# Optimization experiments

Measured on AMD Instinct MI355X. Metric: run time of the kernel, lower is better.

Reference implementation:

```python
import jax, jax.numpy as jnp
import numpy as np

N = 100_000          # nodes
E = 600_000          # directed edges, stored in reverse pairs (2i <-> 2i+1)
D_NODE = 128
D_EDGE = 16
UNITS = 128
EDGE_STEPS = 4
NODE_STEPS = 4


def setup_inputs() -> dict:
    key = jax.random.key(0)
    ks = jax.random.split(key, 10)
    s = 0.05
    # undirected pairs -> both directions so every edge has a reverse edge
    u = jax.random.randint(ks[0], (E // 2,), 0, N, dtype=jnp.int32)
    v = jax.random.randint(ks[1], (E // 2,), 0, N, dtype=jnp.int32)
    edge_src = jnp.stack([u, v], axis=1).reshape(-1)  # [E]
    edge_dst = jnp.stack([v, u], axis=1).reshape(-1)  # [E]
    edge_rev = (jnp.arange(E, dtype=jnp.int32) ^ 1)   # reverse-edge index
    return dict(
        node_feature=jax.random.normal(ks[2], (N, D_NODE), jnp.float32),
        edge_feature=jax.random.normal(ks[3], (E, D_EDGE), jnp.float32),
        W_init=jax.random.normal(ks[4], (D_NODE + D_EDGE, UNITS), jnp.float32) * s,
        b_init=jnp.zeros((UNITS,), jnp.float32),
        W_edge=jax.random.normal(ks[5], (EDGE_STEPS, UNITS, UNITS), jnp.float32) * s,
        b_edge=jnp.zeros((EDGE_STEPS, UNITS), jnp.float32),
        W_gin0=jax.random.normal(ks[6], (D_NODE + UNITS, UNITS), jnp.float32) * s,
        W_gin=jax.random.normal(ks[7], (NODE_STEPS - 1, UNITS, UNITS), jnp.float32) * s,
        b_gin=jnp.zeros((NODE_STEPS, UNITS), jnp.float32),
        eps=jnp.zeros((NODE_STEPS,), jnp.float32),
        edge_src=edge_src,
        edge_dst=edge_dst,
        edge_rev=edge_rev,
    )


def reference(node_feature, edge_feature, W_init, b_init, W_edge, b_edge,
              W_gin0, W_gin, b_gin, eps, edge_src, edge_dst, edge_rev):
    relu = jax.nn.relu
    seg = lambda x: jax.ops.segment_sum(x, edge_dst, num_segments=N)

    # ---- EdgeConv stack (D-MPNN directed edge message passing) ----
    # initial edge state: act(W [x_src || e])
    h = relu(jnp.concatenate([node_feature[edge_src], edge_feature], axis=-1)
             @ W_init + b_init)                                  # [E, U]
    for t in range(EDGE_STEPS):
        agg = seg(h)                                             # [N, U] incoming sums
        m = agg[edge_src] - h[edge_rev]                          # exclude reverse edge
        h = relu(h + m @ W_edge[t] + b_edge[t])                  # residual edge update

    # ---- NodeReadout: sum incoming edge states per node ----
    readout = seg(h)                                             # [N, U]
    x = jnp.concatenate([node_feature, readout], axis=-1)        # [N, D_NODE + U]

    # ---- GINConv stack (use_edge_features=False) ----
    for t in range(NODE_STEPS):
        agg = seg(x[edge_src])                                   # [N, d] neighbor sum
        W = W_gin0 if t == 0 else W_gin[t - 1]
        x = relu(((1.0 + eps[t]) * x + agg) @ W + b_gin[t])      # [N, U]

    return x, h
```

## Files before the change

kernel.cpp:

```cpp
#include <hip/hip_runtime.h>

#define N_NODES 100000
#define N_EDGES 600000
#define SCAN_NB ((N_NODES + 255) / 256)

typedef unsigned short u16;
typedef __attribute__((ext_vector_type(8))) short short8v;
typedef __attribute__((ext_vector_type(4))) short short4v;
typedef __attribute__((ext_vector_type(4))) float f32x4;
typedef __attribute__((ext_vector_type(8))) __bf16 bf16x8v;

__device__ __forceinline__ u16 f2bf(float f) {
  unsigned u = __builtin_bit_cast(unsigned, f);
  unsigned r = (u + 0x7fffu + ((u >> 16) & 1u)) >> 16;
  return (u16)r;
}
__device__ __forceinline__ float bf2f(u16 v) {
  unsigned u = ((unsigned)v) << 16;
  return __builtin_bit_cast(float, u);
}
__device__ __forceinline__ short8v shfl_xor4_v(short8v v) {
  int4 iv = __builtin_bit_cast(int4, v);
  iv.x = __shfl_xor(iv.x, 4, 64);
  iv.y = __shfl_xor(iv.y, 4, 64);
  iv.z = __shfl_xor(iv.z, 4, 64);
  iv.w = __shfl_xor(iv.w, 4, 64);
  return __builtin_bit_cast(short8v, iv);
}

__global__ __launch_bounds__(256) void convert_nf_kernel(const float* __restrict__ nf,
                                                         u16* __restrict__ nfbf) {
  size_t idx = ((size_t)blockIdx.x * 256 + threadIdx.x) * 8;
  if (idx >= (size_t)N_NODES * 128) return;
  float4 a = *(const float4*)(nf + idx);
  float4 b = *(const float4*)(nf + idx + 4);
  short8v o = {(short)f2bf(a.x), (short)f2bf(a.y), (short)f2bf(a.z), (short)f2bf(a.w),
               (short)f2bf(b.x), (short)f2bf(b.y), (short)f2bf(b.z), (short)f2bf(b.w)};
  *(short8v*)(nfbf + idx) = o;
}

__global__ void hist_kernel(const int* __restrict__ dst, int* __restrict__ cnt) {
  int e = blockIdx.x * 256 + threadIdx.x;
  if (e < N_EDGES) atomicAdd(&cnt[dst[e]], 1);
}

__global__ __launch_bounds__(256) void scan1_kernel(int* __restrict__ cnt,
                                                    int* __restrict__ off,
                                                    int* __restrict__ blk) {
  __shared__ int s[256];
  int i = blockIdx.x * 256 + threadIdx.x;
  int v = (i < N_NODES) ? cnt[i] : 0;
  if (i < N_NODES) cnt[i] = 0;
  s[threadIdx.x] = v;
  __syncthreads();
  for (int d = 1; d < 256; d <<= 1) {
    int t = (threadIdx.x >= d) ? s[threadIdx.x - d] : 0;
    __syncthreads();
    s[threadIdx.x] += t;
    __syncthreads();
  }
  if (i < N_NODES) off[i] = s[threadIdx.x] - v;
  if (threadIdx.x == 255) blk[blockIdx.x] = s[255];
}

__global__ __launch_bounds__(512) void scan2_kernel(int* __restrict__ blk) {
  __shared__ int s[512];
  int v = (threadIdx.x < SCAN_NB) ? blk[threadIdx.x] : 0;
  s[threadIdx.x] = v;
  __syncthreads();
  for (int d = 1; d < 512; d <<= 1) {
    int t = (threadIdx.x >= d) ? s[threadIdx.x - d] : 0;
    __syncthreads();
    s[threadIdx.x] += t;
    __syncthreads();
  }
  if (threadIdx.x < SCAN_NB) blk[threadIdx.x] = s[threadIdx.x] - v;
}

__global__ __launch_bounds__(256) void scan3_kernel(int* __restrict__ off,
                                                    const int* __restrict__ blk) {
  int i = blockIdx.x * 256 + threadIdx.x;
  if (i < N_NODES) off[i] += blk[blockIdx.x];
  if (i == 0) off[N_NODES] = N_EDGES;
}

__global__ void fill_kernel(const int* __restrict__ dst, const int* __restrict__ src,
                            const int* __restrict__ off, int* __restrict__ cur,
                            int* __restrict__ csr_e, int* __restrict__ csr_s) {
  int e = blockIdx.x * 256 + threadIdx.x;
  if (e < N_EDGES) {
    int d = dst[e];
    int p = off[d] + atomicAdd(&cur[d], 1);
    csr_e[p] = e;
    csr_s[p] = src[e];
  }
}

__global__ __launch_bounds__(256) void segsum_hbf_kernel(const u16* __restrict__ hbf,
                                                         const int* __restrict__ off,
                                                         const int* __restrict__ csr_e,
                                                         u16* __restrict__ aggb) {
  int node = blockIdx.x * 4 + (threadIdx.x >> 6);
  int l = threadIdx.x & 63;
  int p0 = off[node], p1 = off[node + 1];
  int deg = p1 - p0;
  int e_l = (l < deg) ? csr_e[p0 + min(l, deg - 1)] : 0;
  float a0 = 0.f, a1 = 0.f;
  int jmax = min(deg, 64);
  for (int j = 0; j < jmax; ++j) {
    int e = __shfl(e_l, j, 64);
    unsigned u = *(const unsigned*)(hbf + (size_t)e * 128 + 2 * l);
    a0 += __builtin_bit_cast(float, u << 16);
    a1 += __builtin_bit_cast(float, u & 0xffff0000u);
  }
  for (int p = p0 + 64; p < p1; ++p) {
    int e = csr_e[p];
    unsigned u = *(const unsigned*)(hbf + (size_t)e * 128 + 2 * l);
    a0 += __builtin_bit_cast(float, u << 16);
    a1 += __builtin_bit_cast(float, u & 0xffff0000u);
  }
  unsigned o = (unsigned)f2bf(a0) | (((unsigned)f2bf(a1)) << 16);
  *(unsigned*)(aggb + (size_t)node * 128 + 2 * l) = o;
}

__global__ __launch_bounds__(256) void segsum_readout_kernel(const u16* __restrict__ hbf,
                                                             const int* __restrict__ off,
                                                             const int* __restrict__ csr_e,
                                                             u16* __restrict__ readout) {
  int node = blockIdx.x * 4 + (threadIdx.x >> 6);
  int l = threadIdx.x & 63;
  int p0 = off[node], p1 = off[node + 1];
  int deg = p1 - p0;
  int e_l = (l < deg) ? csr_e[p0 + min(l, deg - 1)] : 0;
  float a0 = 0.f, a1 = 0.f;
  int jmax = min(deg, 64);
  for (int j = 0; j < jmax; ++j) {
    int e = __shfl(e_l, j, 64);
    unsigned u = __builtin_nontemporal_load((const unsigned*)(hbf + (size_t)e * 128 + 2 * l));
    a0 += __builtin_bit_cast(float, u << 16);
    a1 += __builtin_bit_cast(float, u & 0xffff0000u);
  }
  for (int p = p0 + 64; p < p1; ++p) {
    int e = csr_e[p];
    unsigned u = __builtin_nontemporal_load((const unsigned*)(hbf + (size_t)e * 128 + 2 * l));
    a0 += __builtin_bit_cast(float, u << 16);
    a1 += __builtin_bit_cast(float, u & 0xffff0000u);
  }
  unsigned o = (unsigned)f2bf(a0) | (((unsigned)f2bf(a1)) << 16);
  *(unsigned*)(readout + (size_t)node * 128 + 2 * l) = o;
}

#define PREP_INIT 0
#define PREP_EDGE 1
#define PREP_GIN0 2
#define PREP_GINX 3
#define EPI_BR  1
#define EPI_ABR 2

template<int KSTEPS, int PREPM, int EPIM, int OUTBF>
__global__ __launch_bounds__(256, 3) void mfma_gemm(
    const float* __restrict__ Wf, int KREAL,
    const float* __restrict__ bias,
    const void* __restrict__ P0,
    const void* __restrict__ P1,
    const int* __restrict__ srcIdx,
    const int* __restrict__ csr_off,
    const int* __restrict__ csr_s,
    const float* __restrict__ epsp,
    float* __restrict__ OutF32,
    void* __restrict__ Out, int numRows) {
  constexpr int RS = KSTEPS * 32 + 8;
  constexpr bool WLATE = (KSTEPS >= 8);
  __shared__ short amem[64 * RS];
  const int t = threadIdx.x;
  const int l = t & 63;
  const int w = t >> 6;
  const int g = l >> 4;
  const int n0 = l & 15;
  const int base = blockIdx.x * 64;

  short8v wf[KSTEPS][2];
  auto load_w = [&]() {
    #pragma unroll
    for (int s = 0; s < KSTEPS; ++s) {
      #pragma unroll
      for (int ct = 0; ct < 2; ++ct) {
        short8v v;
        #pragma unroll
        for (int j = 0; j < 8; ++j) {
          int k = 32 * s + 8 * g + j;
          float wv = (k < KREAL) ? Wf[(size_t)k * 128 + (2 * w + ct) * 16 + n0] : 0.f;
          v[j] = (short)f2bf(wv);
        }
        wf[s][ct] = v;
      }
    }
  };
  if constexpr (!WLATE) load_w();

  float bb[2];
  #pragma unroll
  for (int ct = 0; ct < 2; ++ct) bb[ct] = bias[(2 * w + ct) * 16 + n0];
  float alpha = 0.f;
  if constexpr (PREPM == PREP_GIN0 || PREPM == PREP_GINX) alpha = 1.f + epsp[0];

  short8v hself[4];

  if constexpr (PREPM == PREP_INIT) {
    const int i = t >> 2, q = t & 3;
    const int row = base + i;
    const int sn = srcIdx[row];
    const u16* nrow = (const u16*)P0 + (size_t)sn * 128 + q * 32;
    #pragma unroll
    for (int c = 0; c < 4; ++c)
      *(short8v*)(&amem[i * RS + q * 32 + 8 * c]) = *(const short8v*)(nrow + 8 * c);
    #pragma unroll
    for (int z = 0; z < 2; ++z) {
      int col = 128 + (2 * q + z) * 4;
      short4v o = {0, 0, 0, 0};
      if (col < 144) {
        float4 vv = *(const float4*)((const float*)P1 + (size_t)row * 16 + (col - 128));
        o = {(short)f2bf(vv.x), (short)f2bf(vv.y), (short)f2bf(vv.z), (short)f2bf(vv.w)};
      }
      *(short4v*)(&amem[i * RS + col]) = o;
    }
  } else if constexpr (PREPM == PREP_EDGE) {
    const int i = t >> 2, q = t & 3;
    const int row = base + i;
    const int sn = srcIdx[row];
    const u16* arow = (const u16*)P0 + (size_t)sn * 128 + q * 32;
    const u16* hrow = (const u16*)P1 + (size_t)row * 128 + q * 32;
    short8v av[4];
    #pragma unroll
    for (int c = 0; c < 4; ++c) av[c] = *(const short8v*)(arow + 8 * c);
    #pragma unroll
    for (int c = 0; c < 4; ++c) hself[c] = *(const short8v*)(hrow + 8 * c);
    #pragma unroll
    for (int c = 0; c < 4; ++c) {
      short8v hrev = shfl_xor4_v(hself[c]);
      short8v o;
      #pragma unroll
      for (int j = 0; j < 8; ++j)
        o[j] = (short)f2bf(bf2f((u16)av[c][j]) - bf2f((u16)hrev[j]));
      *(short8v*)(&amem[i * RS + q * 32 + 8 * c]) = o;
    }
  } else if constexpr (PREPM == PREP_GIN0) {
    const int i2 = t >> 3, q = t & 7;
    #pragma unroll
    for (int half = 0; half < 2; ++half) {
      const int r = i2 + 32 * half;
      const int row = base + r;
      const int n = (row < numRows) ? row : (numRows - 1);
      const int p0 = csr_off[n], p1 = csr_off[n + 1];
      const u16* basep = (q < 4) ? (const u16*)P0 : (const u16*)P1;
      const int coff = (q < 4) ? 32 * q : 32 * (q - 4);
      float acc[32];
      const u16* self = basep + (size_t)n * 128 + coff;
      #pragma unroll
      for (int c8 = 0; c8 < 4; ++c8) {
        short8v v = *(const short8v*)(self + 8 * c8);
        #pragma unroll
        for (int j = 0; j < 8; ++j) acc[8 * c8 + j] = alpha * bf2f((u16)v[j]);
      }
      for (int p = p0; p < p1; ++p) {
        const u16* nb = basep + (size_t)csr_s[p] * 128 + coff;
        #pragma unroll
        for (int c8 = 0; c8 < 4; ++c8) {
          short8v v = *(const short8v*)(nb + 8 * c8);
          #pragma unroll
          for (int j = 0; j < 8; ++j) acc[8 * c8 + j] += bf2f((u16)v[j]);
        }
      }
      #pragma unroll
      for (int c4 = 0; c4 < 8; ++c4) {
        short4v o = {(short)f2bf(acc[4 * c4 + 0]), (short)f2bf(acc[4 * c4 + 1]),
                     (short)f2bf(acc[4 * c4 + 2]), (short)f2bf(acc[4 * c4 + 3])};
        *(short4v*)(&amem[r * RS + 32 * q + 4 * c4]) = o;
      }
    }
  } else {
    const int i = t >> 2, q = t & 3;
    const int row = base + i;
    const int n = (row < numRows) ? row : (numRows - 1);
    const int p0 = csr_off[n], p1 = csr_off[n + 1];
    float acc[32];
    const u16* self = (const u16*)P0 + (size_t)n * 128 + 32 * q;
    #pragma unroll
    for (int c8 = 0; c8 < 4; ++c8) {
      short8v v = *(const short8v*)(self + 8 * c8);
      #pragma unroll
      for (int j = 0; j < 8; ++j) acc[8 * c8 + j] = alpha * bf2f((u16)v[j]);
    }
    for (int p = p0; p < p1; ++p) {
      const u16* nb = (const u16*)P0 + (size_t)csr_s[p] * 128 + 32 * q;
      #pragma unroll
      for (int c8 = 0; c8 < 4; ++c8) {
        short8v v = *(const short8v*)(nb + 8 * c8);
        #pragma unroll
        for (int j = 0; j < 8; ++j) acc[8 * c8 + j] += bf2f((u16)v[j]);
      }
    }
    #pragma unroll
    for (int c4 = 0; c4 < 8; ++c4) {
      short4v o = {(short)f2bf(acc[4 * c4 + 0]), (short)f2bf(acc[4 * c4 + 1]),
                   (short)f2bf(acc[4 * c4 + 2]), (short)f2bf(acc[4 * c4 + 3])};
      *(short4v*)(&amem[i * RS + 32 * q + 4 * c4]) = o;
    }
  }
  __syncthreads();
  if constexpr (WLATE) load_w();

  f32x4 acc[4][2];
  #pragma unroll
  for (int rt = 0; rt < 4; ++rt)
    #pragma unroll
    for (int ct = 0; ct < 2; ++ct) acc[rt][ct] = (f32x4){0.f, 0.f, 0.f, 0.f};
  #pragma unroll
  for (int s = 0; s < KSTEPS; ++s) {
    bf16x8v af[4];
    #pragma unroll
    for (int rt = 0; rt < 4; ++rt) {
      short8v araw = *(const short8v*)(&amem[(16 * rt + n0) * RS + s * 32 + g * 8]);
      af[rt] = __builtin_bit_cast(bf16x8v, araw);
    }
    #pragma unroll
    for (int rt = 0; rt < 4; ++rt)
      #pragma unroll
      for (int ct = 0; ct < 2; ++ct)
        acc[rt][ct] = __builtin_amdgcn_mfma_f32_16x16x32_bf16(
            af[rt], __builtin_bit_cast(bf16x8v, wf[s][ct]), acc[rt][ct], 0, 0, 0);
  }

  if constexpr (EPIM == EPI_ABR) {
    __syncthreads();
    {
      const int i = t >> 2, q = t & 3;
      #pragma unroll
      for (int c = 0; c < 4; ++c)
        *(short8v*)(&amem[i * RS + q * 32 + 8 * c]) = hself[c];
    }
    __syncthreads();
  }

  if constexpr (OUTBF) {
    if constexpr (EPIM != EPI_ABR) __syncthreads();
    #pragma unroll
    for (int rt = 0; rt < 4; ++rt) {
      #pragma unroll
      for (int ct = 0; ct < 2; ++ct) {
        #pragma unroll
        for (int r = 0; r < 4; ++r) {
          int lrow = 16 * rt + 4 * g + r;
          int lcol = (2 * w + ct) * 16 + n0;
          float o = acc[rt][ct][r];
          if constexpr (EPIM == EPI_ABR) o += bf2f((u16)amem[lrow * RS + lcol]);
          o = fmaxf(o + bb[ct], 0.f);
          if constexpr (OUTBF == 2)
            __builtin_nontemporal_store(o, &OutF32[(size_t)(base + lrow) * 128 + lcol]);
          amem[lrow * RS + lcol] = (short)f2bf(o);
        }
      }
    }
    __syncthreads();
    {
      const int i = t >> 2, q = t & 3;
      const int row = base + i;
      if (row < numRows) {
        u16* orow = (u16*)Out + (size_t)row * 128 + q * 32;
        #pragma unroll
        for (int c = 0; c < 4; ++c)
          *(short8v*)(orow + 8 * c) = *(const short8v*)(&amem[i * RS + q * 32 + 8 * c]);
      }
    }
  } else {
    #pragma unroll
    for (int rt = 0; rt < 4; ++rt) {
      #pragma unroll
      for (int ct = 0; ct < 2; ++ct) {
        #pragma unroll
        for (int r = 0; r < 4; ++r) {
          int row = base + 16 * rt + 4 * g + r;
          if (row < numRows) {
            int lrow = 16 * rt + 4 * g + r;
            int lcol = (2 * w + ct) * 16 + n0;
            float o = acc[rt][ct][r];
            if constexpr (EPIM == EPI_ABR) o += bf2f((u16)amem[lrow * RS + lcol]);
            o = fmaxf(o + bb[ct], 0.f);
            __builtin_nontemporal_store(o, &((float*)Out)[(size_t)row * 128 + lcol]);
          }
        }
      }
    }
  }
}

extern "C" void kernel_launch(void* const* d_in, const int* in_sizes, int n_in,
                              void* d_out, int out_size, void* d_ws, size_t ws_size,
                              hipStream_t stream) {
  const float* nf     = (const float*)d_in[0];
  const float* ef     = (const float*)d_in[1];
  const float* W_init = (const float*)d_in[2];
  const float* b_init = (const float*)d_in[3];
  const float* W_edge = (const float*)d_in[4];
  const float* b_edge = (const float*)d_in[5];
  const float* W_gin0 = (const float*)d_in[6];
  const float* W_gin  = (const float*)d_in[7];
  const float* b_gin  = (const float*)d_in[8];
  const float* eps    = (const float*)d_in[9];
  const int* esrc     = (const int*)d_in[10];
  const int* edst     = (const int*)d_in[11];

  float* xout  = (float*)d_out;
  float* h_out = xout + (size_t)N_NODES * 128;

  const size_t NB = (size_t)N_NODES * 128 * 2;
  const size_t EB = (size_t)N_EDGES * 128 * 2;
  char* wsb = (char*)d_ws;
  u16* aggbf   = (u16*)wsb;
  u16* xbf1    = (u16*)wsb;
  u16* hbf     = (u16*)(wsb + NB);
  u16* readout = (u16*)(wsb + NB + EB);
  u16* xbf0    = (u16*)(wsb + 2 * NB + EB);
  u16* nfbf    = (u16*)(wsb + 3 * NB + EB);
  int* csr_off = (int*)(wsb + 4 * NB + EB);
  int* cursor  = csr_off + (N_NODES + 1);
  int* csr_e   = cursor + N_NODES;
  int* csr_s   = csr_e + N_EDGES;
  int* blk     = csr_s + N_EDGES;

  convert_nf_kernel<<<(N_NODES * 128 / 8 + 255) / 256, 256, 0, stream>>>(nf, nfbf);

  hipMemsetAsync(cursor, 0, N_NODES * sizeof(int), stream);
  hist_kernel<<<(N_EDGES + 255) / 256, 256, 0, stream>>>(edst, cursor);
  scan1_kernel<<<SCAN_NB, 256, 0, stream>>>(cursor, csr_off, blk);
  scan2_kernel<<<1, 512, 0, stream>>>(blk);
  scan3_kernel<<<SCAN_NB, 256, 0, stream>>>(csr_off, blk);
  fill_kernel<<<(N_EDGES + 255) / 256, 256, 0, stream>>>(edst, esrc, csr_off, cursor, csr_e, csr_s);

  const int ETILES = N_EDGES / 64;
  const int NTILES = (N_NODES + 63) / 64;

  mfma_gemm<5, PREP_INIT, EPI_BR, 1><<<ETILES, 256, 0, stream>>>(
      W_init, 144, b_init, nfbf, ef, esrc, nullptr, nullptr, nullptr, nullptr, hbf, N_EDGES);

  for (int t = 0; t < 3; ++t) {
    segsum_hbf_kernel<<<N_NODES / 4, 256, 0, stream>>>(hbf, csr_off, csr_e, aggbf);
    mfma_gemm<4, PREP_EDGE, EPI_ABR, 1><<<ETILES, 256, 0, stream>>>(
        W_edge + (size_t)t * 128 * 128, 128, b_edge + (size_t)t * 128,
        aggbf, hbf, esrc, nullptr, nullptr, nullptr, nullptr, hbf, N_EDGES);
  }
  segsum_hbf_kernel<<<N_NODES / 4, 256, 0, stream>>>(hbf, csr_off, csr_e, aggbf);
  mfma_gemm<4, PREP_EDGE, EPI_ABR, 2><<<ETILES, 256, 0, stream>>>(
      W_edge + (size_t)3 * 128 * 128, 128, b_edge + (size_t)3 * 128,
      aggbf, hbf, esrc, nullptr, nullptr, nullptr, h_out, hbf, N_EDGES);

  segsum_readout_kernel<<<N_NODES / 4, 256, 0, stream>>>(hbf, csr_off, csr_e, readout);

  mfma_gemm<8, PREP_GIN0, EPI_BR, 1><<<NTILES, 256, 0, stream>>>(
      W_gin0, 256, b_gin, nfbf, readout, nullptr, csr_off, csr_s, eps, nullptr, xbf0, N_NODES);

  mfma_gemm<4, PREP_GINX, EPI_BR, 1><<<NTILES, 256, 0, stream>>>(
      W_gin, 128, b_gin + 128, xbf0, nullptr, nullptr, csr_off, csr_s, eps + 1, nullptr, xbf1, N_NODES);
  mfma_gemm<4, PREP_GINX, EPI_BR, 1><<<NTILES, 256, 0, stream>>>(
      W_gin + (size_t)128 * 128, 128, b_gin + 256, xbf1, nullptr, nullptr, csr_off, csr_s, eps + 2, nullptr, xbf0, N_NODES);
  mfma_gemm<4, PREP_GINX, EPI_BR, 0><<<NTILES, 256, 0, stream>>>(
      W_gin + (size_t)2 * 128 * 128, 128, b_gin + 384, xbf0, nullptr, nullptr, csr_off, csr_s, eps + 3, nullptr, xout, N_NODES);

  (void)in_sizes; (void)n_in; (void)out_size; (void)ws_size;
}
```

Baseline: 1.178 ms.

## Pre-convert weights to bf16, make GEMM blocks persistent, interleave node feature with readout

A new kernel converts all weight matrices once into a transposed bf16 blob, so each GEMM block loads its weight fragments as vector loads instead of doing strided fp32 loads and conversions. The GEMM kernels now loop over several 64-row tiles per block (5 for edges, 3 for nodes), which spreads the weight-load and bias setup over more rows. Node features and the readout are stored together in one 256-wide row, so the first GIN step gathers 32-column slices of a single interleaved row. The cost is fewer blocks, which lowers parallelism and latency hiding, plus one extra small kernel launch.

```diff
diff --git a/kernel.cpp b/kernel.cpp
--- a/kernel.cpp
+++ b/kernel.cpp
@@ -3,6 +3,12 @@
 #define N_NODES 100000
 #define N_EDGES 600000
 #define SCAN_NB ((N_NODES + 255) / 256)
+
+#define WOFF_I  0
+#define WOFF_E  20480
+#define WOFF_G0 86016
+#define WOFF_G  118784
+#define WTOTAL  167936
 
 typedef unsigned short u16;
 typedef __attribute__((ext_vector_type(8))) short short8v;
@@ -29,14 +35,44 @@
 }
 
 __global__ __launch_bounds__(256) void convert_nf_kernel(const float* __restrict__ nf,
-                                                         u16* __restrict__ nfbf) {
+                                                         u16* __restrict__ nfro) {
   size_t idx = ((size_t)blockIdx.x * 256 + threadIdx.x) * 8;
   if (idx >= (size_t)N_NODES * 128) return;
   float4 a = *(const float4*)(nf + idx);
   float4 b = *(const float4*)(nf + idx + 4);
   short8v o = {(short)f2bf(a.x), (short)f2bf(a.y), (short)f2bf(a.z), (short)f2bf(a.w),
                (short)f2bf(b.x), (short)f2bf(b.y), (short)f2bf(b.z), (short)f2bf(b.w)};
-  *(short8v*)(nfbf + idx) = o;
+  size_t row = idx >> 7, col = idx & 127;
+  *(short8v*)(nfro + row * 256 + col) = o;
+}
+
+__global__ __launch_bounds__(256) void convert_w_kernel(const float* __restrict__ Wi,
+                                                        const float* __restrict__ We,
+                                                        const float* __restrict__ Wg0,
+                                                        const float* __restrict__ Wg,
+                                                        u16* __restrict__ out) {
+  int e = blockIdx.x * 256 + threadIdx.x;
+  if (e >= WTOTAL) return;
+  float v;
+  if (e < WOFF_E) {
+    int col = e / 160, k = e % 160;
+    v = (k < 144) ? Wi[(size_t)k * 128 + col] : 0.f;
+  } else if (e < WOFF_G0) {
+    int r = e - WOFF_E;
+    int m = r / 16384; r %= 16384;
+    int col = r / 128, k = r % 128;
+    v = We[(size_t)m * 16384 + (size_t)k * 128 + col];
+  } else if (e < WOFF_G) {
+    int r = e - WOFF_G0;
+    int col = r / 256, k = r % 256;
+    v = Wg0[(size_t)k * 128 + col];
+  } else {
+    int r = e - WOFF_G;
+    int m = r / 16384; r %= 16384;
+    int col = r / 128, k = r % 128;
+    v = Wg[(size_t)m * 16384 + (size_t)k * 128 + col];
+  }
+  out[e] = f2bf(v);
 }
 
 __global__ void hist_kernel(const int* __restrict__ dst, int* __restrict__ cnt) {
@@ -126,7 +162,7 @@
 __global__ __launch_bounds__(256) void segsum_readout_kernel(const u16* __restrict__ hbf,
                                                              const int* __restrict__ off,
                                                              const int* __restrict__ csr_e,
-                                                             u16* __restrict__ readout) {
+                                                             u16* __restrict__ ro) {
   int node = blockIdx.x * 4 + (threadIdx.x >> 6);
   int l = threadIdx.x & 63;
   int p0 = off[node], p1 = off[node + 1];
@@ -147,7 +183,7 @@
     a1 += __builtin_bit_cast(float, u & 0xffff0000u);
   }
   unsigned o = (unsigned)f2bf(a0) | (((unsigned)f2bf(a1)) << 16);
-  *(unsigned*)(readout + (size_t)node * 128 + 2 * l) = o;
+  *(unsigned*)(ro + (size_t)node * 256 + 2 * l) = o;
 }
 
 #define PREP_INIT 0
@@ -157,9 +193,9 @@
 #define EPI_BR  1
 #define EPI_ABR 2
 
-template<int KSTEPS, int PREPM, int EPIM, int OUTBF>
+template<int KSTEPS, int PREPM, int EPIM, int OUTBF, int TPB>
 __global__ __launch_bounds__(256, 3) void mfma_gemm(
-    const float* __restrict__ Wf, int KREAL,
+    const u16* __restrict__ Wt,
     const float* __restrict__ bias,
     const void* __restrict__ P0,
     const void* __restrict__ P1,
@@ -177,24 +213,14 @@
   const int w = t >> 6;
   const int g = l >> 4;
   const int n0 = l & 15;
-  const int base = blockIdx.x * 64;
 
   short8v wf[KSTEPS][2];
   auto load_w = [&]() {
     #pragma unroll
-    for (int s = 0; s < KSTEPS; ++s) {
-      #pragma unroll
-      for (int ct = 0; ct < 2; ++ct) {
-        short8v v;
-        #pragma unroll
-        for (int j = 0; j < 8; ++j) {
-          int k = 32 * s + 8 * g + j;
-          float wv = (k < KREAL) ? Wf[(size_t)k * 128 + (2 * w + ct) * 16 + n0] : 0.f;
-          v[j] = (short)f2bf(wv);
-        }
-        wf[s][ct] = v;
-      }
-    }
+    for (int s = 0; s < KSTEPS; ++s)
+      #pragma unroll
+      for (int ct = 0; ct < 2; ++ct)
+        wf[s][ct] = *(const short8v*)(Wt + (size_t)((2 * w + ct) * 16 + n0) * (KSTEPS * 32) + 32 * s + 8 * g);
   };
   if constexpr (!WLATE) load_w();
 
@@ -204,58 +230,88 @@
   float alpha = 0.f;
   if constexpr (PREPM == PREP_GIN0 || PREPM == PREP_GINX) alpha = 1.f + epsp[0];
 
-  short8v hself[4];
-
-  if constexpr (PREPM == PREP_INIT) {
-    const int i = t >> 2, q = t & 3;
-    const int row = base + i;
-    const int sn = srcIdx[row];
-    const u16* nrow = (const u16*)P0 + (size_t)sn * 128 + q * 32;
-    #pragma unroll
-    for (int c = 0; c < 4; ++c)
-      *(short8v*)(&amem[i * RS + q * 32 + 8 * c]) = *(const short8v*)(nrow + 8 * c);
-    #pragma unroll
-    for (int z = 0; z < 2; ++z) {
-      int col = 128 + (2 * q + z) * 4;
-      short4v o = {0, 0, 0, 0};
-      if (col < 144) {
-        float4 vv = *(const float4*)((const float*)P1 + (size_t)row * 16 + (col - 128));
-        o = {(short)f2bf(vv.x), (short)f2bf(vv.y), (short)f2bf(vv.z), (short)f2bf(vv.w)};
-      }
-      *(short4v*)(&amem[i * RS + col]) = o;
-    }
-  } else if constexpr (PREPM == PREP_EDGE) {
-    const int i = t >> 2, q = t & 3;
-    const int row = base + i;
-    const int sn = srcIdx[row];
-    const u16* arow = (const u16*)P0 + (size_t)sn * 128 + q * 32;
-    const u16* hrow = (const u16*)P1 + (size_t)row * 128 + q * 32;
-    short8v av[4];
-    #pragma unroll
-    for (int c = 0; c < 4; ++c) av[c] = *(const short8v*)(arow + 8 * c);
-    #pragma unroll
-    for (int c = 0; c < 4; ++c) hself[c] = *(const short8v*)(hrow + 8 * c);
-    #pragma unroll
-    for (int c = 0; c < 4; ++c) {
-      short8v hrev = shfl_xor4_v(hself[c]);
-      short8v o;
-      #pragma unroll
-      for (int j = 0; j < 8; ++j)
-        o[j] = (short)f2bf(bf2f((u16)av[c][j]) - bf2f((u16)hrev[j]));
-      *(short8v*)(&amem[i * RS + q * 32 + 8 * c]) = o;
-    }
-  } else if constexpr (PREPM == PREP_GIN0) {
-    const int i2 = t >> 3, q = t & 7;
-    #pragma unroll
-    for (int half = 0; half < 2; ++half) {
-      const int r = i2 + 32 * half;
-      const int row = base + r;
+  for (int it = 0; it < TPB; ++it) {
+    const int base = (blockIdx.x * TPB + it) * 64;
+    short8v hself[4];
+
+    if constexpr (PREPM == PREP_INIT) {
+      const int i = t >> 2, q = t & 3;
+      const int row = base + i;
+      const int sn = srcIdx[row];
+      const u16* nrow = (const u16*)P0 + (size_t)sn * 256 + q * 32;
+      #pragma unroll
+      for (int c = 0; c < 4; ++c)
+        *(short8v*)(&amem[i * RS + q * 32 + 8 * c]) = *(const short8v*)(nrow + 8 * c);
+      #pragma unroll
+      for (int z = 0; z < 2; ++z) {
+        int col = 128 + (2 * q + z) * 4;
+        short4v o = {0, 0, 0, 0};
+        if (col < 144) {
+          f32x4 vv = __builtin_nontemporal_load(
+              (const f32x4*)((const float*)P1 + (size_t)row * 16 + (col - 128)));
+          o = {(short)f2bf(vv.x), (short)f2bf(vv.y), (short)f2bf(vv.z), (short)f2bf(vv.w)};
+        }
+        *(short4v*)(&amem[i * RS + col]) = o;
+      }
+    } else if constexpr (PREPM == PREP_EDGE) {
+      const int i = t >> 2, q = t & 3;
+      const int row = base + i;
+      const int sn = srcIdx[row];
+      const u16* arow = (const u16*)P0 + (size_t)sn * 128 + q * 32;
+      const u16* hrow = (const u16*)P1 + (size_t)row * 128 + q * 32;
+      short8v av[4];
+      #pragma unroll
+      for (int c = 0; c < 4; ++c) av[c] = *(const short8v*)(arow + 8 * c);
+      #pragma unroll
+      for (int c = 0; c < 4; ++c) hself[c] = *(const short8v*)(hrow + 8 * c);
+      #pragma unroll
+      for (int c = 0; c < 4; ++c) {
+        short8v hrev = shfl_xor4_v(hself[c]);
+        short8v o;
+        #pragma unroll
+        for (int j = 0; j < 8; ++j)
+          o[j] = (short)f2bf(bf2f((u16)av[c][j]) - bf2f((u16)hrev[j]));
+        *(short8v*)(&amem[i * RS + q * 32 + 8 * c]) = o;
+      }
+    } else if constexpr (PREPM == PREP_GIN0) {
+      const int i2 = t >> 3, q = t & 7;
+      #pragma unroll
+      for (int half = 0; half < 2; ++half) {
+        const int r = i2 + 32 * half;
+        const int row = base + r;
+        const int n = (row < numRows) ? row : (numRows - 1);
+        const int p0 = csr_off[n], p1 = csr_off[n + 1];
+        float acc[32];
+        const u16* self = (const u16*)P0 + (size_t)n * 256 + 32 * q;
+        #pragma unroll
+        for (int c8 = 0; c8 < 4; ++c8) {
+          short8v v = *(const short8v*)(self + 8 * c8);
+          #pragma unroll
+          for (int j = 0; j < 8; ++j) acc[8 * c8 + j] = alpha * bf2f((u16)v[j]);
+        }
+        for (int p = p0; p < p1; ++p) {
+          const u16* nb = (const u16*)P0 + (size_t)csr_s[p] * 256 + 32 * q;
+          #pragma unroll
+          for (int c8 = 0; c8 < 4; ++c8) {
+            short8v v = *(const short8v*)(nb + 8 * c8);
+            #pragma unroll
+            for (int j = 0; j < 8; ++j) acc[8 * c8 + j] += bf2f((u16)v[j]);
+          }
+        }
+        #pragma unroll
+        for (int c4 = 0; c4 < 8; ++c4) {
+          short4v o = {(short)f2bf(acc[4 * c4 + 0]), (short)f2bf(acc[4 * c4 + 1]),
+                       (short)f2bf(acc[4 * c4 + 2]), (short)f2bf(acc[4 * c4 + 3])};
+          *(short4v*)(&amem[r * RS + 32 * q + 4 * c4]) = o;
+        }
+      }
+    } else {
+      const int i = t >> 2, q = t & 3;
+      const int row = base + i;
       const int n = (row < numRows) ? row : (numRows - 1);
       const int p0 = csr_off[n], p1 = csr_off[n + 1];
-      const u16* basep = (q < 4) ? (const u16*)P0 : (const u16*)P1;
-      const int coff = (q < 4) ? 32 * q : 32 * (q - 4);
       float acc[32];
-      const u16* self = basep + (size_t)n * 128 + coff;
+      const u16* self = (const u16*)P0 + (size_t)n * 128 + 32 * q;
       #pragma unroll
       for (int c8 = 0; c8 < 4; ++c8) {
         short8v v = *(const short8v*)(self + 8 * c8);
@@ -263,7 +319,7 @@
         for (int j = 0; j < 8; ++j) acc[8 * c8 + j] = alpha * bf2f((u16)v[j]);
       }
       for (int p = p0; p < p1; ++p) {
-        const u16* nb = basep + (size_t)csr_s[p] * 128 + coff;
+        const u16* nb = (const u16*)P0 + (size_t)csr_s[p] * 128 + 32 * q;
         #pragma unroll
         for (int c8 = 0; c8 < 4; ++c8) {
           short8v v = *(const short8v*)(nb + 8 * c8);
@@ -275,122 +331,93 @@
       for (int c4 = 0; c4 < 8; ++c4) {
         short4v o = {(short)f2bf(acc[4 * c4 + 0]), (short)f2bf(acc[4 * c4 + 1]),
                      (short)f2bf(acc[4 * c4 + 2]), (short)f2bf(acc[4 * c4 + 3])};
-        *(short4v*)(&amem[r * RS + 32 * q + 4 * c4]) = o;
+        *(short4v*)(&amem[i * RS + 32 * q + 4 * c4]) = o;
       }
     }
-  } else {
-    const int i = t >> 2, q = t & 3;
-    const int row = base + i;
-    const int n = (row < numRows) ? row : (numRows - 1);
-    const int p0 = csr_off[n], p1 = csr_off[n + 1];
-    float acc[32];
-    const u16* self = (const u16*)P0 + (size_t)n * 128 + 32 * q;
-    #pragma unroll
-    for (int c8 = 0; c8 < 4; ++c8) {
-      short8v v = *(const short8v*)(self + 8 * c8);
-      #pragma unroll
-      for (int j = 0; j < 8; ++j) acc[8 * c8 + j] = alpha * bf2f((u16)v[j]);
-    }
-    for (int p = p0; p < p1; ++p) {
-      const u16* nb = (const u16*)P0 + (size_t)csr_s[p] * 128 + 32 * q;
-      #pragma unroll
-      for (int c8 = 0; c8 < 4; ++c8) {
-        short8v v = *(const short8v*)(nb + 8 * c8);
-        #pragma unroll
-        for (int j = 0; j < 8; ++j) acc[8 * c8 + j] += bf2f((u16)v[j]);
-      }
-    }
-    #pragma unroll
-    for (int c4 = 0; c4 < 8; ++c4) {
-      short4v o = {(short)f2bf(acc[4 * c4 + 0]), (short)f2bf(acc[4 * c4 + 1]),
-                   (short)f2bf(acc[4 * c4 + 2]), (short)f2bf(acc[4 * c4 + 3])};
-      *(short4v*)(&amem[i * RS + 32 * q + 4 * c4]) = o;
-    }
-  }
-  __syncthreads();
-  if constexpr (WLATE) load_w();
-
-  f32x4 acc[4][2];
-  #pragma unroll
-  for (int rt = 0; rt < 4; ++rt)
-    #pragma unroll
-    for (int ct = 0; ct < 2; ++ct) acc[rt][ct] = (f32x4){0.f, 0.f, 0.f, 0.f};
-  #pragma unroll
-  for (int s = 0; s < KSTEPS; ++s) {
-    bf16x8v af[4];
-    #pragma unroll
-    for (int rt = 0; rt < 4; ++rt) {
-      short8v araw = *(const short8v*)(&amem[(16 * rt + n0) * RS + s * 32 + g * 8]);
-      af[rt] = __builtin_bit_cast(bf16x8v, araw);
-    }
+    __syncthreads();
+    if constexpr (WLATE) load_w();
+
+    f32x4 acc[4][2];
     #pragma unroll
     for (int rt = 0; rt < 4; ++rt)
       #pragma unroll
-      for (int ct = 0; ct < 2; ++ct)
-        acc[rt][ct] = __builtin_amdgcn_mfma_f32_16x16x32_bf16(
-            af[rt], __builtin_bit_cast(bf16x8v, wf[s][ct]), acc[rt][ct], 0, 0, 0);
-  }
-
-  if constexpr (EPIM == EPI_ABR) {
-    __syncthreads();
-    {
-      const int i = t >> 2, q = t & 3;
-      #pragma unroll
-      for (int c = 0; c < 4; ++c)
-        *(short8v*)(&amem[i * RS + q * 32 + 8 * c]) = hself[c];
+      for (int ct = 0; ct < 2; ++ct) acc[rt][ct] = (f32x4){0.f, 0.f, 0.f, 0.f};
+    #pragma unroll
+    for (int s = 0; s < KSTEPS; ++s) {
+      bf16x8v af[4];
+      #pragma unroll
+      for (int rt = 0; rt < 4; ++rt) {
+        short8v araw = *(const short8v*)(&amem[(16 * rt + n0) * RS + s * 32 + g * 8]);
+        af[rt] = __builtin_bit_cast(bf16x8v, araw);
+      }
+      #pragma unroll
+      for (int rt = 0; rt < 4; ++rt)
+        #pragma unroll
+        for (int ct = 0; ct < 2; ++ct)
+          acc[rt][ct] = __builtin_amdgcn_mfma_f32_16x16x32_bf16(
+              af[rt], __builtin_bit_cast(bf16x8v, wf[s][ct]), acc[rt][ct], 0, 0, 0);
     }
-    __syncthreads();
-  }
-
-  if constexpr (OUTBF) {
-    if constexpr (EPIM != EPI_ABR) __syncthreads();
-    #pragma unroll
-    for (int rt = 0; rt < 4; ++rt) {
-      #pragma unroll
-      for (int ct = 0; ct < 2; ++ct) {
-        #pragma unroll
-        for (int r = 0; r < 4; ++r) {
-          int lrow = 16 * rt + 4 * g + r;
-          int lcol = (2 * w + ct) * 16 + n0;
-          float o = acc[rt][ct][r];
-          if constexpr (EPIM == EPI_ABR) o += bf2f((u16)amem[lrow * RS + lcol]);
-          o = fmaxf(o + bb[ct], 0.f);
-          if constexpr (OUTBF == 2)
-            __builtin_nontemporal_store(o, &OutF32[(size_t)(base + lrow) * 128 + lcol]);
-          amem[lrow * RS + lcol] = (short)f2bf(o);
-        }
-      }
+
+    if constexpr (EPIM == EPI_ABR) {
+      __syncthreads();
+      {
+        const int i = t >> 2, q = t & 3;
+        #pragma unroll
+        for (int c = 0; c < 4; ++c)
+          *(short8v*)(&amem[i * RS + q * 32 + 8 * c]) = hself[c];
+      }
+      __syncthreads();
     }
-    __syncthreads();
-    {
-      const int i = t >> 2, q = t & 3;
-      const int row = base + i;
-      if (row < numRows) {
-        u16* orow = (u16*)Out + (size_t)row * 128 + q * 32;
-        #pragma unroll
-        for (int c = 0; c < 4; ++c)
-          *(short8v*)(orow + 8 * c) = *(const short8v*)(&amem[i * RS + q * 32 + 8 * c]);
-      }
-    }
-  } else {
-    #pragma unroll
-    for (int rt = 0; rt < 4; ++rt) {
-      #pragma unroll
-      for (int ct = 0; ct < 2; ++ct) {
-        #pragma unroll
-        for (int r = 0; r < 4; ++r) {
-          int row = base + 16 * rt + 4 * g + r;
-          if (row < numRows) {
+
+    if constexpr (OUTBF) {
+      if constexpr (EPIM != EPI_ABR) __syncthreads();
+      #pragma unroll
+      for (int rt = 0; rt < 4; ++rt) {
+        #pragma unroll
+        for (int ct = 0; ct < 2; ++ct) {
+          #pragma unroll
+          for (int r = 0; r < 4; ++r) {
             int lrow = 16 * rt + 4 * g + r;
             int lcol = (2 * w + ct) * 16 + n0;
             float o = acc[rt][ct][r];
             if constexpr (EPIM == EPI_ABR) o += bf2f((u16)amem[lrow * RS + lcol]);
             o = fmaxf(o + bb[ct], 0.f);
-            __builtin_nontemporal_store(o, &((float*)Out)[(size_t)row * 128 + lcol]);
+            if constexpr (OUTBF == 2)
+              __builtin_nontemporal_store(o, &OutF32[(size_t)(base + lrow) * 128 + lcol]);
+            amem[lrow * RS + lcol] = (short)f2bf(o);
           }
         }
       }
+      __syncthreads();
+      {
+        const int i = t >> 2, q = t & 3;
+        const int row = base + i;
+        if (row < numRows) {
+          u16* orow = (u16*)Out + (size_t)row * 128 + q * 32;
+          #pragma unroll
+          for (int c = 0; c < 4; ++c)
+            *(short8v*)(orow + 8 * c) = *(const short8v*)(&amem[i * RS + q * 32 + 8 * c]);
+        }
+      }
+    } else {
+      #pragma unroll
+      for (int rt = 0; rt < 4; ++rt) {
+        #pragma unroll
+        for (int ct = 0; ct < 2; ++ct) {
+          #pragma unroll
+          for (int r = 0; r < 4; ++r) {
+            int row = base + 16 * rt + 4 * g + r;
+            if (row < numRows) {
+              int lcol = (2 * w + ct) * 16 + n0;
+              float o = acc[rt][ct][r];
+              o = fmaxf(o + bb[ct], 0.f);
+              __builtin_nontemporal_store(o, &((float*)Out)[(size_t)row * 128 + lcol]);
+            }
+          }
+        }
+      }
     }
+    __syncthreads();
   }
 }
 
@@ -419,16 +446,17 @@
   u16* aggbf   = (u16*)wsb;
   u16* xbf1    = (u16*)wsb;
   u16* hbf     = (u16*)(wsb + NB);
-  u16* readout = (u16*)(wsb + NB + EB);
-  u16* xbf0    = (u16*)(wsb + 2 * NB + EB);
-  u16* nfbf    = (u16*)(wsb + 3 * NB + EB);
+  u16* nfro    = (u16*)(wsb + NB + EB);
+  u16* xbf0    = (u16*)(wsb + 3 * NB + EB);
   int* csr_off = (int*)(wsb + 4 * NB + EB);
   int* cursor  = csr_off + (N_NODES + 1);
   int* csr_e   = cursor + N_NODES;
   int* csr_s   = csr_e + N_EDGES;
   int* blk     = csr_s + N_EDGES;
-
-  convert_nf_kernel<<<(N_NODES * 128 / 8 + 255) / 256, 256, 0, stream>>>(nf, nfbf);
+  u16* wblob   = (u16*)(blk + SCAN_NB + 1);
+
+  convert_nf_kernel<<<(N_NODES * 128 / 8 + 255) / 256, 256, 0, stream>>>(nf, nfro);
+  convert_w_kernel<<<(WTOTAL + 255) / 256, 256, 0, stream>>>(W_init, W_edge, W_gin0, W_gin, wblob);
 
   hipMemsetAsync(cursor, 0, N_NODES * sizeof(int), stream);
   hist_kernel<<<(N_EDGES + 255) / 256, 256, 0, stream>>>(edst, cursor);
@@ -437,34 +465,36 @@
   scan3_kernel<<<SCAN_NB, 256, 0, stream>>>(csr_off, blk);
   fill_kernel<<<(N_EDGES + 255) / 256, 256, 0, stream>>>(edst, esrc, csr_off, cursor, csr_e, csr_s);
 
-  const int ETILES = N_EDGES / 64;
-  const int NTILES = (N_NODES + 63) / 64;
-
-  mfma_gemm<5, PREP_INIT, EPI_BR, 1><<<ETILES, 256, 0, stream>>>(
-      W_init, 144, b_init, nfbf, ef, esrc, nullptr, nullptr, nullptr, nullptr, hbf, N_EDGES);
+  const u16* wt_init = wblob + WOFF_I;
+  const u16* wt_edge = wblob + WOFF_E;
+  const u16* wt_gin0 = wblob + WOFF_G0;
+  const u16* wt_gin  = wblob + WOFF_G;
+
+  mfma_gemm<5, PREP_INIT, EPI_BR, 1, 5><<<1875, 256, 0, stream>>>(
+      wt_init, b_init, nfro, ef, esrc, nullptr, nullptr, nullptr, nullptr, hbf, N_EDGES);
 
   for (int t = 0; t < 3; ++t) {
     segsum_hbf_kernel<<<N_NODES / 4, 256, 0, stream>>>(hbf, csr_off, csr_e, aggbf);
-    mfma_gemm<4, PREP_EDGE, EPI_ABR, 1><<<ETILES, 256, 0, stream>>>(
-        W_edge + (size_t)t * 128 * 128, 128, b_edge + (size_t)t * 128,
+    mfma_gemm<4, PREP_EDGE, EPI_ABR, 1, 5><<<1875, 256, 0, stream>>>(
+        wt_edge + (size_t)t * 16384, b_edge + (size_t)t * 128,
         aggbf, hbf, esrc, nullptr, nullptr, nullptr, nullptr, hbf, N_EDGES);
   }
   segsum_hbf_kernel<<<N_NODES / 4, 256, 0, stream>>>(hbf, csr_off, csr_e, aggbf);
-  mfma_gemm<4, PREP_EDGE, EPI_ABR, 2><<<ETILES, 256, 0, stream>>>(
-      W_edge + (size_t)3 * 128 * 128, 128, b_edge + (size_t)3 * 128,
+  mfma_gemm<4, PREP_EDGE, EPI_ABR, 2, 5><<<1875, 256, 0, stream>>>(
+      wt_edge + (size_t)3 * 16384, b_edge + (size_t)3 * 128,
       aggbf, hbf, esrc, nullptr, nullptr, nullptr, h_out, hbf, N_EDGES);
 
-  segsum_readout_kernel<<<N_NODES / 4, 256, 0, stream>>>(hbf, csr_off, csr_e, readout);
-
-  mfma_gemm<8, PREP_GIN0, EPI_BR, 1><<<NTILES, 256, 0, stream>>>(
-      W_gin0, 256, b_gin, nfbf, readout, nullptr, csr_off, csr_s, eps, nullptr, xbf0, N_NODES);
-
-  mfma_gemm<4, PREP_GINX, EPI_BR, 1><<<NTILES, 256, 0, stream>>>(
-      W_gin, 128, b_gin + 128, xbf0, nullptr, nullptr, csr_off, csr_s, eps + 1, nullptr, xbf1, N_NODES);
-  mfma_gemm<4, PREP_GINX, EPI_BR, 1><<<NTILES, 256, 0, stream>>>(
-      W_gin + (size_t)128 * 128, 128, b_gin + 256, xbf1, nullptr, nullptr, csr_off, csr_s, eps + 2, nullptr, xbf0, N_NODES);
-  mfma_gemm<4, PREP_GINX, EPI_BR, 0><<<NTILES, 256, 0, stream>>>(
-      W_gin + (size_t)2 * 128 * 128, 128, b_gin + 384, xbf0, nullptr, nullptr, csr_off, csr_s, eps + 3, nullptr, xout, N_NODES);
+  segsum_readout_kernel<<<N_NODES / 4, 256, 0, stream>>>(hbf, csr_off, csr_e, nfro + 128);
+
+  mfma_gemm<8, PREP_GIN0, EPI_BR, 1, 3><<<521, 256, 0, stream>>>(
+      wt_gin0, b_gin, nfro, nullptr, nullptr, csr_off, csr_s, eps, nullptr, xbf0, N_NODES);
+
+  mfma_gemm<4, PREP_GINX, EPI_BR, 1, 3><<<521, 256, 0, stream>>>(
+      wt_gin, b_gin + 128, xbf0, nullptr, nullptr, csr_off, csr_s, eps + 1, nullptr, xbf1, N_NODES);
+  mfma_gemm<4, PREP_GINX, EPI_BR, 1, 3><<<521, 256, 0, stream>>>(
+      wt_gin + 16384, b_gin + 256, xbf1, nullptr, nullptr, csr_off, csr_s, eps + 2, nullptr, xbf0, N_NODES);
+  mfma_gemm<4, PREP_GINX, EPI_BR, 0, 3><<<521, 256, 0, stream>>>(
+      wt_gin + 2 * 16384, b_gin + 384, xbf0, nullptr, nullptr, csr_off, csr_s, eps + 3, nullptr, xout, N_NODES);
 
   (void)in_sizes; (void)n_in; (void)out_size; (void)ws_size;
 }
```

Measured after the change: 1.111 ms. -5.7%, faster.
